# Kernel optimization log

Measured on AMD Instinct MI355X. Metric: run time of the kernel, lower is better.

## Reference

```python
import jax, jax.numpy as jnp
import numpy as np

ALPHA = 0.2          # LeakyReLU negative slope
NEG_INF = -9e15      # masking value from the original module


def setup_inputs() -> dict:
    key = jax.random.key(0)
    kw, ka, k1, k2, k3 = jax.random.split(key, 5)
    B, N1, N2, F, O = 4, 2048, 2048, 256, 256
    word = jax.random.normal(kw, (B, N2, F), dtype=jnp.float32)
    # 0/1 hypergraph incidence matrix (float, as in the torch module)
    adj = jax.random.randint(ka, (B, N1, N2), 0, 2).astype(jnp.float32)
    stdv = 1.0 / np.sqrt(O)
    W1 = jax.random.uniform(k1, (F, O), jnp.float32, -stdv, stdv)
    W2 = jax.random.uniform(k2, (F, O), jnp.float32, -stdv, stdv)
    w3 = jax.random.uniform(k3, (2 * O, 1), jnp.float32, -stdv, stdv)
    return {"word": word, "adj": adj, "W1": W1, "W2": W2, "w3": w3}


def reference(word, adj, W1, W2, w3):
    # word: [B, N2, F]; adj: [B, N1, N2]; W1/W2: [F, O]; w3: [2O, 1]
    O = W1.shape[1]
    # mean-pool neighbor features per hyperedge (row-normalized adj)
    deg = jnp.sum(adj, axis=-1, keepdims=True)                 # [B, N1, 1]
    deg = jnp.where(deg > 0, deg, jnp.ones_like(deg))
    mp = jnp.matmul(adj / deg, word)                           # [B, N1, F]
    # The original builds 4D tensors h1[b,i,j,:] = adj[b,i,j]*word[b,j,:] and
    # h_mp[b,i,j,:] = adj[b,i,j]*mp[b,i,:], projects both and dots with w3.
    # Since scaling commutes with the linear maps, the scalar score is
    #   adj[b,i,j] * (word[b,j] @ W1 @ w3_a + mp[b,i] @ W2 @ w3_b)
    w3a = w3[:O, 0]                                            # pairs with w1h
    w3b = w3[O:, 0]                                            # pairs with w2h
    s1 = jnp.einsum('bnf,fo,o->bn', word, W1, w3a)             # [B, N2]
    s2 = jnp.einsum('bnf,fo,o->bn', mp, W2, w3b)               # [B, N1]
    pre = adj * (s2[:, :, None] + s1[:, None, :])              # [B, N1, N2]
    alpha = jnp.exp(jax.nn.leaky_relu(pre, ALPHA))
    attention = jnp.where(adj > 0, alpha, NEG_INF)
    attention_edge = jax.nn.softmax(attention, axis=2)         # over N2
    edge = jnp.matmul(attention_edge, word)                    # [B, N1, F]
    return edge
```

## Files before the change

### kernel.cpp

```cpp
#include <hip/hip_runtime.h>

#define B 4
#define N 2048
#define F 256
#define O 256
#define LOG2E 1.4426950408889634f
#define NEG_BIG -9000000000000000.0f

typedef _Float16 f16;
typedef f16 f16x8 __attribute__((ext_vector_type(8)));
typedef float f32x16 __attribute__((ext_vector_type(16)));

#define WS_V1 0
#define WS_V2 256
#define WS_T1 512
#define WS_T2 (512 + B*N)
#define WS_S2 (512 + 2*B*N)
#define WS_CR (512 + 3*B*N)
#define WS_WN (512 + 4*B*N)
#define WT_OFF (1u << 20)
#define MK_OFF (6u << 20)

__device__ __forceinline__ float alpha_of(float pre2) {
  return __builtin_amdgcn_exp2f(fmaxf(pre2, 0.2f * pre2));
}

__global__ __launch_bounds__(256) void k_v(const float* __restrict__ W1,
                                           const float* __restrict__ W2,
                                           const float* __restrict__ w3,
                                           float* __restrict__ ws) {
  int tid = threadIdx.x;
  int lane = tid & 63;
  int f = blockIdx.x * 4 + (tid >> 6);
  float a = 0.f, b = 0.f;
  #pragma unroll
  for (int k = 0; k < 4; ++k) {
    int o = lane + 64 * k;
    a += W1[f * O + o] * w3[o];
    b += W2[f * O + o] * w3[O + o];
  }
  #pragma unroll
  for (int off = 32; off > 0; off >>= 1) {
    a += __shfl_down(a, off);
    b += __shfl_down(b, off);
  }
  if (lane == 0) {
    ws[WS_V1 + f] = a;
    ws[WS_V2 + f] = b;
  }
}

__global__ __launch_bounds__(256) void k_prep(const float* __restrict__ word,
                                              float* __restrict__ ws,
                                              f16* __restrict__ wordT) {
  __shared__ float v1s[F], v2s[F];
  __shared__ __align__(16) f16 tile[F][40];
  int t = threadIdx.x;
  int k0 = blockIdx.x * 32;
  int b = blockIdx.y;

  if (t < 64)       ((float4*)v1s)[t]      = ((const float4*)(ws + WS_V1))[t];
  else if (t < 128) ((float4*)v2s)[t - 64] = ((const float4*)(ws + WS_V2))[t - 64];
  __syncthreads();

  int r = t >> 3;
  int cg = t & 7;
  const float* wrow = word + ((size_t)(b * N + k0 + r)) * F;
  float a = 0.f, bb = 0.f;
  #pragma unroll
  for (int i = 0; i < 8; ++i) {
    int c = i * 32 + cg * 4;
    float4 w = *(const float4*)(wrow + c);
    float4 x1 = *(const float4*)(v1s + c);
    float4 x2 = *(const float4*)(v2s + c);
    a  += w.x * x1.x + w.y * x1.y + w.z * x1.z + w.w * x1.w;
    bb += w.x * x2.x + w.y * x2.y + w.z * x2.z + w.w * x2.w;
    tile[c + 0][r] = (f16)w.x;
    tile[c + 1][r] = (f16)w.y;
    tile[c + 2][r] = (f16)w.z;
    tile[c + 3][r] = (f16)w.w;
  }
  #pragma unroll
  for (int off = 4; off > 0; off >>= 1) {
    a  += __shfl_down(a, off);
    bb += __shfl_down(bb, off);
  }
  if (cg == 0) {
    ws[WS_T1 + b * N + k0 + r] = a * LOG2E;
    ws[WS_T2 + b * N + k0 + r] = bb;
  }
  __syncthreads();

  size_t base = (size_t)b * F * N;
  #pragma unroll
  for (int i = 0; i < 4; ++i) {
    int idx = t + 256 * i;
    int ft = idx >> 7, c = (idx >> 6) & 1, l = idx & 63;
    int f = ft * 32 + (l & 31);
    int rr = c * 16 + ((l >> 5) * 8);
    f16x8 h = *(const f16x8*)&tile[f][rr];
    *(f16x8*)(wordT + base + ((size_t)((ft * 128 + (k0 >> 4) + c) * 64 + l)) * 8) = h;
  }
}

__global__ __launch_bounds__(256) void k_stats(const float* __restrict__ adj,
                                               float* __restrict__ ws,
                                               unsigned char* __restrict__ mask) {
  int row = blockIdx.x;
  int b = row >> 11;
  int t = threadIdx.x;
  int wid = t >> 6, lane = t & 63;
  const float* arow = adj + (size_t)row * N;
  const float* t1b = ws + WS_T1 + b * N;
  const float* t2b = ws + WS_T2 + b * N;

  float4 a0 = *(const float4*)(arow + t * 8);
  float4 a1 = *(const float4*)(arow + t * 8 + 4);
  float4 u0 = *(const float4*)(t2b + t * 8);
  float4 u1 = *(const float4*)(t2b + t * 8 + 4);
  float deg = a0.x + a0.y + a0.z + a0.w + a1.x + a1.y + a1.z + a1.w;
  float dot = a0.x * u0.x + a0.y * u0.y + a0.z * u0.z + a0.w * u0.w +
              a1.x * u1.x + a1.y * u1.y + a1.z * u1.z + a1.w * u1.w;
  unsigned mb = (a0.x > 0.f ? 1u : 0u) | (a0.y > 0.f ? 2u : 0u) |
                (a0.z > 0.f ? 4u : 0u) | (a0.w > 0.f ? 8u : 0u) |
                (a1.x > 0.f ? 16u : 0u) | (a1.y > 0.f ? 32u : 0u) |
                (a1.z > 0.f ? 64u : 0u) | (a1.w > 0.f ? 128u : 0u);
  mask[(size_t)row * 256 + t] = (unsigned char)mb;

  #pragma unroll
  for (int off = 32; off > 0; off >>= 1) {
    deg += __shfl_down(deg, off);
    dot += __shfl_down(dot, off);
  }
  __shared__ float rd[4], rt[4], rm[4], rz[4];
  if (lane == 0) { rd[wid] = deg; rt[wid] = dot; }
  __syncthreads();
  deg = rd[0] + rd[1] + rd[2] + rd[3];
  dot = rt[0] + rt[1] + rt[2] + rt[3];
  float degc = deg > 0.f ? deg : 1.f;
  float s2p = (dot / degc) * LOG2E;

  float4 p0 = *(const float4*)(t1b + t * 8);
  float4 p1 = *(const float4*)(t1b + t * 8 + 4);
  float al[8];
  al[0] = (mb & 1)   ? alpha_of(p0.x + s2p) : NEG_BIG;
  al[1] = (mb & 2)   ? alpha_of(p0.y + s2p) : NEG_BIG;
  al[2] = (mb & 4)   ? alpha_of(p0.z + s2p) : NEG_BIG;
  al[3] = (mb & 8)   ? alpha_of(p0.w + s2p) : NEG_BIG;
  al[4] = (mb & 16)  ? alpha_of(p1.x + s2p) : NEG_BIG;
  al[5] = (mb & 32)  ? alpha_of(p1.y + s2p) : NEG_BIG;
  al[6] = (mb & 64)  ? alpha_of(p1.z + s2p) : NEG_BIG;
  al[7] = (mb & 128) ? alpha_of(p1.w + s2p) : NEG_BIG;
  float m = NEG_BIG;
  #pragma unroll
  for (int j = 0; j < 8; ++j) m = fmaxf(m, al[j]);
  #pragma unroll
  for (int off = 32; off > 0; off >>= 1) m = fmaxf(m, __shfl_down(m, off));
  if (lane == 0) rm[wid] = m;
  __syncthreads();
  m = fmaxf(fmaxf(rm[0], rm[1]), fmaxf(rm[2], rm[3]));

  float negmL = -m * LOG2E;
  float z = 0.f;
  #pragma unroll
  for (int j = 0; j < 8; ++j) z += __builtin_amdgcn_exp2f(fmaf(al[j], LOG2E, negmL));
  #pragma unroll
  for (int off = 32; off > 0; off >>= 1) z += __shfl_down(z, off);
  if (lane == 0) rz[wid] = z;
  __syncthreads();
  if (t == 0) {
    z = rz[0] + rz[1] + rz[2] + rz[3];
    ws[WS_S2 + row] = s2p;
    if (deg > 0.f) {
      ws[WS_CR + row] = negmL - log2f(z);
      ws[WS_WN + row] = 0.f;
    } else {
      ws[WS_CR + row] = 0.f;
      ws[WS_WN + row] = 1.0f / (float)N;
    }
  }
}

__global__ __launch_bounds__(256, 2) void k_gemm(const f16* __restrict__ wordT,
                                                 const unsigned char* __restrict__ maskg,
                                                 const float* __restrict__ ws,
                                                 float* __restrict__ out) {
  __shared__ __align__(16) f16 Aw[2][8][512];
  __shared__ __align__(16) float t1S[N];
  __shared__ float sSC[96];

  const int t = threadIdx.x;
  const int rb = blockIdx.x >> 1, fh = blockIdx.x & 1;
  const int row0 = rb * 32;
  const int b = row0 >> 11;

  *(float4*)&t1S[t * 8]     = *(const float4*)(ws + WS_T1 + b * N + t * 8);
  *(float4*)&t1S[t * 8 + 4] = *(const float4*)(ws + WS_T1 + b * N + t * 8 + 4);
  if (t < 32) {
    sSC[t]      = ws[WS_S2 + row0 + t];
    sSC[32 + t] = ws[WS_CR + row0 + t];
    sSC[64 + t] = ws[WS_WN + row0 + t];
  }
  __syncthreads();

  const int gl = t & 63;
  const int gp = t >> 6;
  const int koff = (gl >> 5) * 8;
  const int rowL = gl & 31;
  const float rs2 = sSC[rowL], rcr = sSC[32 + rowL], rwn = sSC[64 + rowL];
  const unsigned* mrow = (const unsigned*)(maskg + (size_t)(row0 + rowL) * 256);

  const int lw = t & 63;
  const int wv = t >> 6;
  const int ftile = fh * 4 + wv;
  const int fcol = ftile * 32 + (lw & 31);
  const f16* wtb = wordT + (size_t)b * F * N;

  f32x16 acc = {0.f,0.f,0.f,0.f,0.f,0.f,0.f,0.f,0.f,0.f,0.f,0.f,0.f,0.f,0.f,0.f};

  #define GENW(IT, BUF, MW)                                                    \
    {                                                                          \
      const int kb = (IT) * 128 + gp * 32 + koff;                              \
      const float4 ta0 = *(const float4*)&t1S[kb];                             \
      const float4 ta1 = *(const float4*)&t1S[kb + 4];                         \
      const float4 tb0 = *(const float4*)&t1S[kb + 16];                        \
      const float4 tb1 = *(const float4*)&t1S[kb + 20];                        \
      const float ta[8] = {ta0.x, ta0.y, ta0.z, ta0.w, ta1.x, ta1.y, ta1.z, ta1.w}; \
      const float tb[8] = {tb0.x, tb0.y, tb0.z, tb0.w, tb1.x, tb1.y, tb1.z, tb1.w}; \
      const unsigned m0 = (MW) >> koff;                                        \
      const unsigned m1 = (MW) >> (16 + koff);                                 \
      f16x8 h0, h1;                                                            \
      _Pragma("unroll")                                                        \
      for (int j = 0; j < 8; ++j) {                                            \
        float p0 = ta[j] + rs2;                                                \
        float a0v = __builtin_amdgcn_exp2f(fmaxf(p0, 0.2f * p0));              \
        float w0 = ((m0 >> j) & 1u) ? __builtin_amdgcn_exp2f(fmaf(a0v, LOG2E, rcr)) : rwn; \
        h0[j] = (f16)w0;                                                       \
        float p1 = tb[j] + rs2;                                                \
        float a1v = __builtin_amdgcn_exp2f(fmaxf(p1, 0.2f * p1));              \
        float w1 = ((m1 >> j) & 1u) ? __builtin_amdgcn_exp2f(fmaf(a1v, LOG2E, rcr)) : rwn; \
        h1[j] = (f16)w1;                                                       \
      }                                                                        \
      *(f16x8*)&Aw[BUF][gp * 2][gl * 8]     = h0;                              \
      *(f16x8*)&Aw[BUF][gp * 2 + 1][gl * 8] = h1;                              \
    }

  f16x8 bf[8];
  {
    const f16* bp = wtb + ((size_t)(ftile * 128) * 64 + lw) * 8;
    #pragma unroll
    for (int c = 0; c < 8; ++c) bf[c] = *(const f16x8*)(bp + (size_t)c * 512);
  }
  {
    unsigned mw0 = mrow[gp];
    GENW(0, 0, mw0)
  }
  __syncthreads();

  #pragma unroll 2
  for (int it = 0; it < 16; ++it) {
    const int cur = it & 1;
    f16x8 bfn[8];
    if (it < 15) {
      const f16* bp = wtb + ((size_t)(ftile * 128 + (it + 1) * 8) * 64 + lw) * 8;
      #pragma unroll
      for (int c = 0; c < 8; ++c) bfn[c] = *(const f16x8*)(bp + (size_t)c * 512);
      unsigned mwn = mrow[(it + 1) * 4 + gp];
      GENW(it + 1, cur ^ 1, mwn)
    }

    #pragma unroll
    for (int c = 0; c < 8; ++c) {
      const f16x8 af = *(const f16x8*)&Aw[cur][c][lw * 8];
      acc = __builtin_amdgcn_mfma_f32_32x32x16_f16(af, bf[c], acc, 0, 0, 0);
    }
    __syncthreads();

    if (it < 15) {
      #pragma unroll
      for (int c = 0; c < 8; ++c) bf[c] = bfn[c];
    }
  }

  #pragma unroll
  for (int reg = 0; reg < 16; ++reg) {
    int lr = (reg & 3) + 8 * (reg >> 2) + 4 * (lw >> 5);
    out[(size_t)(row0 + lr) * F + fcol] = acc[reg];
  }
}

extern "C" void kernel_launch(void* const* d_in, const int* in_sizes, int n_in,
                              void* d_out, int out_size, void* d_ws, size_t ws_size,
                              hipStream_t stream) {
  const float* word = (const float*)d_in[0];
  const float* adj  = (const float*)d_in[1];
  const float* W1   = (const float*)d_in[2];
  const float* W2   = (const float*)d_in[3];
  const float* w3   = (const float*)d_in[4];
  float* out = (float*)d_out;
  float* ws  = (float*)d_ws;
  f16* wordT = (f16*)((char*)d_ws + WT_OFF);
  unsigned char* mask = (unsigned char*)d_ws + MK_OFF;

  k_v<<<64, 256, 0, stream>>>(W1, W2, w3, ws);
  k_prep<<<dim3(N / 32, B), 256, 0, stream>>>(word, ws, wordT);
  k_stats<<<B * N, 256, 0, stream>>>(adj, ws, mask);
  k_gemm<<<(B * N) / 32 * 2, 256, 0, stream>>>(wordT, mask, ws, out);
}
```

Baseline: 134.0 us.

## Materialize normalized fp16 attention weights in stats kernel; simplify GEMM to pure MFMA

The stats kernel now handles 8 rows per block, one wave per row, using only wave-level reductions. It computes the final normalized softmax weights and writes them as fp16 in the MFMA A-fragment layout, replacing the per-row scalars and bitmask. The GEMM kernel no longer recomputes the exponentials per tile. It streams the precomputed A and B fragments straight from global memory into MFMA, with a swizzled block order. This removes redundant transcendental work from the GEMM, since each weight was being recomputed by both F halves. The cost is about 32 MB of extra fp16 weight traffic, and the GEMM loses its LDS double buffering.

```diff
diff --git a/kernel.cpp b/kernel.cpp
--- a/kernel.cpp
+++ b/kernel.cpp
@@ -8,6 +8,7 @@
 #define NEG_BIG -9000000000000000.0f
 
 typedef _Float16 f16;
+typedef f16 f16x4 __attribute__((ext_vector_type(4)));
 typedef f16 f16x8 __attribute__((ext_vector_type(8)));
 typedef float f32x16 __attribute__((ext_vector_type(16)));
 
@@ -15,11 +16,8 @@
 #define WS_V2 256
 #define WS_T1 512
 #define WS_T2 (512 + B*N)
-#define WS_S2 (512 + 2*B*N)
-#define WS_CR (512 + 3*B*N)
-#define WS_WN (512 + 4*B*N)
 #define WT_OFF (1u << 20)
-#define MK_OFF (6u << 20)
+#define WGT_OFF (8u << 20)
 
 __device__ __forceinline__ float alpha_of(float pre2) {
   return __builtin_amdgcn_exp2f(fmaxf(pre2, 0.2f * pre2));
@@ -103,188 +101,122 @@
   }
 }
 
-__global__ __launch_bounds__(256) void k_stats(const float* __restrict__ adj,
-                                               float* __restrict__ ws,
-                                               unsigned char* __restrict__ mask) {
-  int row = blockIdx.x;
+__global__ __launch_bounds__(512) void k_weights(const float* __restrict__ adj,
+                                                 const float* __restrict__ ws,
+                                                 f16* __restrict__ Wt) {
+  __shared__ __align__(16) f16 tile[8][2056];
+  int t = threadIdx.x;
+  int wid = t >> 6, l = t & 63;
+  int a = blockIdx.x;
+  int row = a * 8 + wid;
   int b = row >> 11;
-  int t = threadIdx.x;
-  int wid = t >> 6, lane = t & 63;
   const float* arow = adj + (size_t)row * N;
   const float* t1b = ws + WS_T1 + b * N;
   const float* t2b = ws + WS_T2 + b * N;
 
-  float4 a0 = *(const float4*)(arow + t * 8);
-  float4 a1 = *(const float4*)(arow + t * 8 + 4);
-  float4 u0 = *(const float4*)(t2b + t * 8);
-  float4 u1 = *(const float4*)(t2b + t * 8 + 4);
-  float deg = a0.x + a0.y + a0.z + a0.w + a1.x + a1.y + a1.z + a1.w;
-  float dot = a0.x * u0.x + a0.y * u0.y + a0.z * u0.z + a0.w * u0.w +
-              a1.x * u1.x + a1.y * u1.y + a1.z * u1.z + a1.w * u1.w;
-  unsigned mb = (a0.x > 0.f ? 1u : 0u) | (a0.y > 0.f ? 2u : 0u) |
-                (a0.z > 0.f ? 4u : 0u) | (a0.w > 0.f ? 8u : 0u) |
-                (a1.x > 0.f ? 16u : 0u) | (a1.y > 0.f ? 32u : 0u) |
-                (a1.z > 0.f ? 64u : 0u) | (a1.w > 0.f ? 128u : 0u);
-  mask[(size_t)row * 256 + t] = (unsigned char)mb;
-
+  float deg = 0.f, dot = 0.f;
+  unsigned mb = 0u;
+  #pragma unroll
+  for (int i = 0; i < 8; ++i) {
+    int k = i * 256 + l * 4;
+    float4 av = *(const float4*)(arow + k);
+    float4 uv = *(const float4*)(t2b + k);
+    deg += av.x + av.y + av.z + av.w;
+    dot += av.x * uv.x + av.y * uv.y + av.z * uv.z + av.w * uv.w;
+    mb |= (av.x > 0.f ? (1u << (4 * i))     : 0u) |
+          (av.y > 0.f ? (1u << (4 * i + 1)) : 0u) |
+          (av.z > 0.f ? (1u << (4 * i + 2)) : 0u) |
+          (av.w > 0.f ? (1u << (4 * i + 3)) : 0u);
+  }
   #pragma unroll
   for (int off = 32; off > 0; off >>= 1) {
-    deg += __shfl_down(deg, off);
-    dot += __shfl_down(dot, off);
-  }
-  __shared__ float rd[4], rt[4], rm[4], rz[4];
-  if (lane == 0) { rd[wid] = deg; rt[wid] = dot; }
-  __syncthreads();
-  deg = rd[0] + rd[1] + rd[2] + rd[3];
-  dot = rt[0] + rt[1] + rt[2] + rt[3];
+    deg += __shfl_xor(deg, off);
+    dot += __shfl_xor(dot, off);
+  }
   float degc = deg > 0.f ? deg : 1.f;
   float s2p = (dot / degc) * LOG2E;
 
-  float4 p0 = *(const float4*)(t1b + t * 8);
-  float4 p1 = *(const float4*)(t1b + t * 8 + 4);
-  float al[8];
-  al[0] = (mb & 1)   ? alpha_of(p0.x + s2p) : NEG_BIG;
-  al[1] = (mb & 2)   ? alpha_of(p0.y + s2p) : NEG_BIG;
-  al[2] = (mb & 4)   ? alpha_of(p0.z + s2p) : NEG_BIG;
-  al[3] = (mb & 8)   ? alpha_of(p0.w + s2p) : NEG_BIG;
-  al[4] = (mb & 16)  ? alpha_of(p1.x + s2p) : NEG_BIG;
-  al[5] = (mb & 32)  ? alpha_of(p1.y + s2p) : NEG_BIG;
-  al[6] = (mb & 64)  ? alpha_of(p1.z + s2p) : NEG_BIG;
-  al[7] = (mb & 128) ? alpha_of(p1.w + s2p) : NEG_BIG;
+  float al[32];
   float m = NEG_BIG;
   #pragma unroll
-  for (int j = 0; j < 8; ++j) m = fmaxf(m, al[j]);
-  #pragma unroll
-  for (int off = 32; off > 0; off >>= 1) m = fmaxf(m, __shfl_down(m, off));
-  if (lane == 0) rm[wid] = m;
-  __syncthreads();
-  m = fmaxf(fmaxf(rm[0], rm[1]), fmaxf(rm[2], rm[3]));
+  for (int i = 0; i < 8; ++i) {
+    int k = i * 256 + l * 4;
+    float4 pv = *(const float4*)(t1b + k);
+    float p0 = pv.x + s2p, p1 = pv.y + s2p, p2 = pv.z + s2p, p3 = pv.w + s2p;
+    al[4 * i + 0] = ((mb >> (4 * i + 0)) & 1u) ? alpha_of(p0) : NEG_BIG;
+    al[4 * i + 1] = ((mb >> (4 * i + 1)) & 1u) ? alpha_of(p1) : NEG_BIG;
+    al[4 * i + 2] = ((mb >> (4 * i + 2)) & 1u) ? alpha_of(p2) : NEG_BIG;
+    al[4 * i + 3] = ((mb >> (4 * i + 3)) & 1u) ? alpha_of(p3) : NEG_BIG;
+    m = fmaxf(m, fmaxf(fmaxf(al[4 * i], al[4 * i + 1]), fmaxf(al[4 * i + 2], al[4 * i + 3])));
+  }
+  #pragma unroll
+  for (int off = 32; off > 0; off >>= 1) m = fmaxf(m, __shfl_xor(m, off));
 
   float negmL = -m * LOG2E;
   float z = 0.f;
   #pragma unroll
-  for (int j = 0; j < 8; ++j) z += __builtin_amdgcn_exp2f(fmaf(al[j], LOG2E, negmL));
-  #pragma unroll
-  for (int off = 32; off > 0; off >>= 1) z += __shfl_down(z, off);
-  if (lane == 0) rz[wid] = z;
+  for (int j = 0; j < 32; ++j) {
+    float e = __builtin_amdgcn_exp2f(fmaf(al[j], LOG2E, negmL));
+    z += e;
+    al[j] = e;
+  }
+  #pragma unroll
+  for (int off = 32; off > 0; off >>= 1) z += __shfl_xor(z, off);
+  float sc, wn;
+  if (deg > 0.f) { sc = 1.0f / z; wn = 0.f; }
+  else           { sc = 0.f;      wn = 1.0f / (float)N; }
+
+  #pragma unroll
+  for (int i = 0; i < 8; ++i) {
+    f16x4 h;
+    #pragma unroll
+    for (int c = 0; c < 4; ++c) {
+      int j = 4 * i + c;
+      float w = ((mb >> j) & 1u) ? al[j] * sc : wn;
+      h[c] = (f16)w;
+    }
+    *(f16x4*)&tile[wid][i * 256 + l * 4] = h;
+  }
   __syncthreads();
-  if (t == 0) {
-    z = rz[0] + rz[1] + rz[2] + rz[3];
-    ws[WS_S2 + row] = s2p;
-    if (deg > 0.f) {
-      ws[WS_CR + row] = negmL - log2f(z);
-      ws[WS_WN + row] = 0.f;
-    } else {
-      ws[WS_CR + row] = 0.f;
-      ws[WS_WN + row] = 1.0f / (float)N;
-    }
-  }
-}
-
-__global__ __launch_bounds__(256, 2) void k_gemm(const f16* __restrict__ wordT,
-                                                 const unsigned char* __restrict__ maskg,
-                                                 const float* __restrict__ ws,
-                                                 float* __restrict__ out) {
-  __shared__ __align__(16) f16 Aw[2][8][512];
-  __shared__ __align__(16) float t1S[N];
-  __shared__ float sSC[96];
-
-  const int t = threadIdx.x;
-  const int rb = blockIdx.x >> 1, fh = blockIdx.x & 1;
-  const int row0 = rb * 32;
-  const int b = row0 >> 11;
-
-  *(float4*)&t1S[t * 8]     = *(const float4*)(ws + WS_T1 + b * N + t * 8);
-  *(float4*)&t1S[t * 8 + 4] = *(const float4*)(ws + WS_T1 + b * N + t * 8 + 4);
-  if (t < 32) {
-    sSC[t]      = ws[WS_S2 + row0 + t];
-    sSC[32 + t] = ws[WS_CR + row0 + t];
-    sSC[64 + t] = ws[WS_WN + row0 + t];
-  }
-  __syncthreads();
-
-  const int gl = t & 63;
-  const int gp = t >> 6;
-  const int koff = (gl >> 5) * 8;
-  const int rowL = gl & 31;
-  const float rs2 = sSC[rowL], rcr = sSC[32 + rowL], rwn = sSC[64 + rowL];
-  const unsigned* mrow = (const unsigned*)(maskg + (size_t)(row0 + rowL) * 256);
-
-  const int lw = t & 63;
-  const int wv = t >> 6;
-  const int ftile = fh * 4 + wv;
-  const int fcol = ftile * 32 + (lw & 31);
-  const f16* wtb = wordT + (size_t)b * F * N;
+
+  size_t base16 = (size_t)(a >> 2) * (128 * 64) + 8 * (a & 3);
+  #pragma unroll
+  for (int s = 0; s < 4; ++s) {
+    int u = s * 512 + t;
+    int r8 = u & 7, half = (u >> 3) & 1, kc = u >> 4;
+    f16x8 v = *(const f16x8*)&tile[r8][kc * 16 + half * 8];
+    *(f16x8*)(Wt + (base16 + (size_t)kc * 64 + half * 32 + r8) * 8) = v;
+  }
+}
+
+__global__ __launch_bounds__(512) void k_gemm(const f16* __restrict__ Wt,
+                                              const f16* __restrict__ wordT,
+                                              float* __restrict__ out) {
+  int bid = blockIdx.x;
+  int sbid = (bid & 7) * 32 + (bid >> 3);
+  int rb2 = sbid >> 1, fh = sbid & 1;
+  int t = threadIdx.x;
+  int wid = t >> 6, l = t & 63;
+  int r32 = rb2 * 2 + (wid >> 2);
+  int ftile = fh * 4 + (wid & 3);
+  int b = r32 >> 6;
+
+  const f16* ap = Wt + (size_t)r32 * (128 * 512) + l * 8;
+  const f16* bp = wordT + (size_t)b * (F * N) + (size_t)ftile * (128 * 512) + l * 8;
 
   f32x16 acc = {0.f,0.f,0.f,0.f,0.f,0.f,0.f,0.f,0.f,0.f,0.f,0.f,0.f,0.f,0.f,0.f};
-
-  #define GENW(IT, BUF, MW)                                                    \
-    {                                                                          \
-      const int kb = (IT) * 128 + gp * 32 + koff;                              \
-      const float4 ta0 = *(const float4*)&t1S[kb];                             \
-      const float4 ta1 = *(const float4*)&t1S[kb + 4];                         \
-      const float4 tb0 = *(const float4*)&t1S[kb + 16];                        \
-      const float4 tb1 = *(const float4*)&t1S[kb + 20];                        \
-      const float ta[8] = {ta0.x, ta0.y, ta0.z, ta0.w, ta1.x, ta1.y, ta1.z, ta1.w}; \
-      const float tb[8] = {tb0.x, tb0.y, tb0.z, tb0.w, tb1.x, tb1.y, tb1.z, tb1.w}; \
-      const unsigned m0 = (MW) >> koff;                                        \
-      const unsigned m1 = (MW) >> (16 + koff);                                 \
-      f16x8 h0, h1;                                                            \
-      _Pragma("unroll")                                                        \
-      for (int j = 0; j < 8; ++j) {                                            \
-        float p0 = ta[j] + rs2;                                                \
-        float a0v = __builtin_amdgcn_exp2f(fmaxf(p0, 0.2f * p0));              \
-        float w0 = ((m0 >> j) & 1u) ? __builtin_amdgcn_exp2f(fmaf(a0v, LOG2E, rcr)) : rwn; \
-        h0[j] = (f16)w0;                                                       \
-        float p1 = tb[j] + rs2;                                                \
-        float a1v = __builtin_amdgcn_exp2f(fmaxf(p1, 0.2f * p1));              \
-        float w1 = ((m1 >> j) & 1u) ? __builtin_amdgcn_exp2f(fmaf(a1v, LOG2E, rcr)) : rwn; \
-        h1[j] = (f16)w1;                                                       \
-      }                                                                        \
-      *(f16x8*)&Aw[BUF][gp * 2][gl * 8]     = h0;                              \
-      *(f16x8*)&Aw[BUF][gp * 2 + 1][gl * 8] = h1;                              \
-    }
-
-  f16x8 bf[8];
-  {
-    const f16* bp = wtb + ((size_t)(ftile * 128) * 64 + lw) * 8;
-    #pragma unroll
-    for (int c = 0; c < 8; ++c) bf[c] = *(const f16x8*)(bp + (size_t)c * 512);
-  }
-  {
-    unsigned mw0 = mrow[gp];
-    GENW(0, 0, mw0)
-  }
-  __syncthreads();
-
-  #pragma unroll 2
-  for (int it = 0; it < 16; ++it) {
-    const int cur = it & 1;
-    f16x8 bfn[8];
-    if (it < 15) {
-      const f16* bp = wtb + ((size_t)(ftile * 128 + (it + 1) * 8) * 64 + lw) * 8;
-      #pragma unroll
-      for (int c = 0; c < 8; ++c) bfn[c] = *(const f16x8*)(bp + (size_t)c * 512);
-      unsigned mwn = mrow[(it + 1) * 4 + gp];
-      GENW(it + 1, cur ^ 1, mwn)
-    }
-
-    #pragma unroll
-    for (int c = 0; c < 8; ++c) {
-      const f16x8 af = *(const f16x8*)&Aw[cur][c][lw * 8];
-      acc = __builtin_amdgcn_mfma_f32_32x32x16_f16(af, bf[c], acc, 0, 0, 0);
-    }
-    __syncthreads();
-
-    if (it < 15) {
-      #pragma unroll
-      for (int c = 0; c < 8; ++c) bf[c] = bfn[c];
-    }
-  }
-
+  #pragma unroll 8
+  for (int c = 0; c < 128; ++c) {
+    f16x8 af = *(const f16x8*)(ap + (size_t)c * 512);
+    f16x8 bf = *(const f16x8*)(bp + (size_t)c * 512);
+    acc = __builtin_amdgcn_mfma_f32_32x32x16_f16(af, bf, acc, 0, 0, 0);
+  }
+
+  int row0 = r32 * 32;
+  int fcol = ftile * 32 + (l & 31);
   #pragma unroll
   for (int reg = 0; reg < 16; ++reg) {
-    int lr = (reg & 3) + 8 * (reg >> 2) + 4 * (lw >> 5);
+    int lr = (reg & 3) + 8 * (reg >> 2) + 4 * (l >> 5);
     out[(size_t)(row0 + lr) * F + fcol] = acc[reg];
   }
 }
@@ -300,10 +232,10 @@
   float* out = (float*)d_out;
   float* ws  = (float*)d_ws;
   f16* wordT = (f16*)((char*)d_ws + WT_OFF);
-  unsigned char* mask = (unsigned char*)d_ws + MK_OFF;
+  f16* Wt    = (f16*)((char*)d_ws + WGT_OFF);
 
   k_v<<<64, 256, 0, stream>>>(W1, W2, w3, ws);
   k_prep<<<dim3(N / 32, B), 256, 0, stream>>>(word, ws, wordT);
-  k_stats<<<B * N, 256, 0, stream>>>(adj, ws, mask);
-  k_gemm<<<(B * N) / 32 * 2, 256, 0, stream>>>(wordT, mask, ws, out);
-}
+  k_weights<<<(B * N) / 8, 512, 0, stream>>>(adj, ws, Wt);
+  k_gemm<<<256, 512, 0, stream>>>(Wt, wordT, out);
+}
```

Result: slower. 143.7 us (+7.2%).
